# Kernel tuning notes

Hardware: AMD Instinct MI355X
Metric: run time of the kernel (lower is better)

The kernel has to match this reference:

```python
import jax, jax.numpy as jnp
import numpy as np

D_MODEL = 1024
D_STATE = 64
CHUNK = 256
BATCH = 4
SEQ_LEN = 4096


def setup_inputs() -> dict:
    key = jax.random.key(0)
    k1, k2, k3, k4, k5 = jax.random.split(key, 5)
    u = jax.random.normal(k1, (BATCH, SEQ_LEN, D_MODEL), jnp.float32)
    delta = jax.random.uniform(k2, (BATCH, SEQ_LEN, D_MODEL), jnp.float32)
    B = jax.random.normal(k3, (BATCH, SEQ_LEN, D_STATE), jnp.float32)
    C = jax.random.normal(k4, (BATCH, SEQ_LEN, D_STATE), jnp.float32)
    # matches nn.init.uniform_(A_log, -3.0, -1.0)
    A_log = jax.random.uniform(k5, (D_STATE, D_MODEL), jnp.float32, minval=-3.0, maxval=-1.0)
    return {"u": u, "delta": delta, "B": B, "C": C, "A_log": A_log}


def reference(u, delta, B, C, A_log):
    # delta is accepted but unused, as in the original forward.
    batch, seq_len, d_model = u.shape
    d_state = A_log.shape[0]
    n_chunks = seq_len // CHUNK  # seq_len chosen divisible by chunk_size
    A = -jnp.exp(A_log)  # (N, D)

    # Split sequence into chunks; hidden state resets at each chunk boundary,
    # so all chunks scan independently (vectorized over the n_chunks axis).
    # time-major layout for lax.scan: (CHUNK, batch, n_chunks, ...)
    uc = jnp.moveaxis(u.reshape(batch, n_chunks, CHUNK, d_model), 2, 0)
    Bc = jnp.moveaxis(B.reshape(batch, n_chunks, CHUNK, d_state), 2, 0)
    Cc = jnp.moveaxis(C.reshape(batch, n_chunks, CHUNK, d_state), 2, 0)

    h0 = jnp.zeros((batch, n_chunks, d_state, d_model), u.dtype)

    def step(h, inp):
        x_t, B_t, C_t = inp  # (b,c,D), (b,c,N), (b,c,N)
        h = A * h + B_t[..., :, None] * x_t[..., None, :]  # (b,c,N,D)
        y = jnp.einsum('bcn,bcnd->bcd', C_t, h)             # (b,c,D)
        return h, y

    _, ys = jax.lax.scan(step, h0, (uc, Bc, Cc))  # (CHUNK, b, n_chunks, D)
    out = jnp.moveaxis(ys, 0, 2).reshape(batch, seq_len, d_model)
    return out
```

## Files before the change

kernel.cpp:

```cpp
#include <hip/hip_runtime.h>

typedef float v4 __attribute__((ext_vector_type(4)));

#define D_MODEL 1024
#define D_STATE 64
#define CHUNK   256
#define TILE_T  64

__global__ __launch_bounds__(256, 4)
void YvParallelScan_kernel(const float* __restrict__ u,
                           const float* __restrict__ B,
                           const float* __restrict__ C,
                           const float* __restrict__ A_log,
                           float* __restrict__ out) {
    __shared__ v4 sB[TILE_T * 16];
    __shared__ v4 sC[TILE_T * 16];

    const int bid = blockIdx.x;
    const int bc  = bid >> 4;
    const int ds  = bid & 15;
    const int tid = threadIdx.x;
    const int ng  = tid & 3;
    const int dq  = tid >> 2;
    const int d   = ds * 64 + dq;
    const int rowbase = bc * CHUNK;

    const v4* Bg = (const v4*)(B + (size_t)rowbase * D_STATE);
    const v4* Cg = (const v4*)(C + (size_t)rowbase * D_STATE);

    float a[16], h[16];
#pragma unroll
    for (int j = 0; j < 16; ++j) {
        const int n = ng * 16 + j;
        a[j] = -__expf(A_log[n * D_MODEL + d]);
        h[j] = 0.f;
    }

    const float* uptr = u + (size_t)rowbase * D_MODEL + d;
    float*       optr = out + (size_t)rowbase * D_MODEL + d;

    float xa = uptr[0];
    float xb = uptr[D_MODEL];

    for (int ti = 0; ti < CHUNK / TILE_T; ++ti) {
#pragma unroll
        for (int k = 0; k < 4; ++k) {
            sB[k * 256 + tid] = Bg[ti * 1024 + k * 256 + tid];
            sC[k * 256 + tid] = Cg[ti * 1024 + k * 256 + tid];
        }
        __syncthreads();

#pragma unroll 4
        for (int tl = 0; tl < TILE_T; ++tl) {
            const int t  = ti * TILE_T + tl;
            const int tp = (t + 2 < CHUNK) ? (t + 2) : (CHUNK - 1);
            const float xn = uptr[(size_t)tp * D_MODEL];

            const float x = xa;
            float acc0 = 0.f, acc1 = 0.f;
#pragma unroll
            for (int jj = 0; jj < 4; ++jj) {
                const v4 b4 = sB[tl * 16 + ng * 4 + jj];
                const v4 c4 = sC[tl * 16 + ng * 4 + jj];
#pragma unroll
                for (int k = 0; k < 4; ++k) {
                    const int j = jj * 4 + k;
                    h[j] = a[j] * h[j] + b4[k] * x;
                    if (k & 1) acc1 += c4[k] * h[j];
                    else       acc0 += c4[k] * h[j];
                }
            }
            float acc = acc0 + acc1;
            acc += __shfl_xor(acc, 1);
            acc += __shfl_xor(acc, 2);
            if (ng == 0) optr[(size_t)t * D_MODEL] = acc;
            xa = xb; xb = xn;
        }
        __syncthreads();
    }
}

extern "C" void kernel_launch(void* const* d_in, const int* in_sizes, int n_in,
                              void* d_out, int out_size, void* d_ws, size_t ws_size,
                              hipStream_t stream) {
    const float* u     = (const float*)d_in[0];
    const float* B     = (const float*)d_in[2];
    const float* C     = (const float*)d_in[3];
    const float* A_log = (const float*)d_in[4];
    float* out = (float*)d_out;

    YvParallelScan_kernel<<<1024, 256, 0, stream>>>(u, B, C, A_log, out);
}
```

Baseline: 259.6 us.

## Process two d-channels per thread and stream B/C from registers instead of LDS

Each thread now handles two adjacent model channels, so every B/C element read is reused across two state recurrences. Shared-memory staging and block barriers are removed: B and C values are loaded straight from global memory into registers and double-buffered one timestep ahead. The grid is halved to 512 blocks and launch bounds drop to 2 waves-per-EU to fit the extra registers. This trades lower occupancy and fewer blocks (less parallelism across CUs) for fewer barriers, fewer LDS reads and vectorized u/out accesses.

```diff
diff --git a/kernel.cpp b/kernel.cpp
--- a/kernel.cpp
+++ b/kernel.cpp
@@ -1,82 +1,111 @@
 #include <hip/hip_runtime.h>
 
 typedef float v4 __attribute__((ext_vector_type(4)));
+typedef float v2 __attribute__((ext_vector_type(2)));
 
 #define D_MODEL 1024
 #define D_STATE 64
 #define CHUNK   256
-#define TILE_T  64
 
-__global__ __launch_bounds__(256, 4)
+__global__ __launch_bounds__(256, 2)
 void YvParallelScan_kernel(const float* __restrict__ u,
                            const float* __restrict__ B,
                            const float* __restrict__ C,
                            const float* __restrict__ A_log,
                            float* __restrict__ out) {
-    __shared__ v4 sB[TILE_T * 16];
-    __shared__ v4 sC[TILE_T * 16];
-
     const int bid = blockIdx.x;
-    const int bc  = bid >> 4;
-    const int ds  = bid & 15;
+    const int bc  = bid >> 3;
+    const int dsl = bid & 7;
     const int tid = threadIdx.x;
     const int ng  = tid & 3;
-    const int dq  = tid >> 2;
-    const int d   = ds * 64 + dq;
+    const int dp  = tid >> 2;
+    const int d   = dsl * 128 + dp * 2;
     const int rowbase = bc * CHUNK;
 
-    const v4* Bg = (const v4*)(B + (size_t)rowbase * D_STATE);
-    const v4* Cg = (const v4*)(C + (size_t)rowbase * D_STATE);
-
-    float a[16], h[16];
+    float a0[16], a1[16], h0[16], h1[16];
 #pragma unroll
     for (int j = 0; j < 16; ++j) {
         const int n = ng * 16 + j;
-        a[j] = -__expf(A_log[n * D_MODEL + d]);
-        h[j] = 0.f;
+        v2 al = *(const v2*)(A_log + (size_t)n * D_MODEL + d);
+        a0[j] = -__expf(al[0]);
+        a1[j] = -__expf(al[1]);
+        h0[j] = 0.f; h1[j] = 0.f;
     }
 
-    const float* uptr = u + (size_t)rowbase * D_MODEL + d;
+    const v4* Bg = (const v4*)(B + (size_t)rowbase * D_STATE) + ng * 4;
+    const v4* Cg = (const v4*)(C + (size_t)rowbase * D_STATE) + ng * 4;
+    const float* uptr = u   + (size_t)rowbase * D_MODEL + d;
     float*       optr = out + (size_t)rowbase * D_MODEL + d;
 
-    float xa = uptr[0];
-    float xb = uptr[D_MODEL];
+    v2 x0 = *(const v2*)(uptr);
+    v2 x1 = *(const v2*)(uptr + D_MODEL);
 
-    for (int ti = 0; ti < CHUNK / TILE_T; ++ti) {
+    v4 bA[4], cA[4], bB[4], cB[4];
 #pragma unroll
-        for (int k = 0; k < 4; ++k) {
-            sB[k * 256 + tid] = Bg[ti * 1024 + k * 256 + tid];
-            sC[k * 256 + tid] = Cg[ti * 1024 + k * 256 + tid];
-        }
-        __syncthreads();
+    for (int jj = 0; jj < 4; ++jj) { bA[jj] = Bg[jj]; cA[jj] = Cg[jj]; }
 
-#pragma unroll 4
-        for (int tl = 0; tl < TILE_T; ++tl) {
-            const int t  = ti * TILE_T + tl;
-            const int tp = (t + 2 < CHUNK) ? (t + 2) : (CHUNK - 1);
-            const float xn = uptr[(size_t)tp * D_MODEL];
+    for (int t = 0; t < CHUNK; t += 2) {
+        {
+#pragma unroll
+            for (int jj = 0; jj < 4; ++jj) {
+                bB[jj] = Bg[(size_t)(t + 1) * 16 + jj];
+                cB[jj] = Cg[(size_t)(t + 1) * 16 + jj];
+            }
+            const int tp = (t + 2 < CHUNK) ? t + 2 : CHUNK - 1;
+            const v2 xn = *(const v2*)(uptr + (size_t)tp * D_MODEL);
 
-            const float x = xa;
             float acc0 = 0.f, acc1 = 0.f;
 #pragma unroll
             for (int jj = 0; jj < 4; ++jj) {
-                const v4 b4 = sB[tl * 16 + ng * 4 + jj];
-                const v4 c4 = sC[tl * 16 + ng * 4 + jj];
+                const v4 b = bA[jj], c = cA[jj];
 #pragma unroll
                 for (int k = 0; k < 4; ++k) {
                     const int j = jj * 4 + k;
-                    h[j] = a[j] * h[j] + b4[k] * x;
-                    if (k & 1) acc1 += c4[k] * h[j];
-                    else       acc0 += c4[k] * h[j];
+                    h0[j] = a0[j] * h0[j] + b[k] * x0[0];
+                    h1[j] = a1[j] * h1[j] + b[k] * x0[1];
+                    acc0 += c[k] * h0[j];
+                    acc1 += c[k] * h1[j];
                 }
             }
-            float acc = acc0 + acc1;
-            acc += __shfl_xor(acc, 1);
-            acc += __shfl_xor(acc, 2);
-            if (ng == 0) optr[(size_t)t * D_MODEL] = acc;
-            xa = xb; xb = xn;
+            acc0 += __shfl_xor(acc0, 1); acc0 += __shfl_xor(acc0, 2);
+            acc1 += __shfl_xor(acc1, 1); acc1 += __shfl_xor(acc1, 2);
+            if (ng == 0) {
+                v2 o; o[0] = acc0; o[1] = acc1;
+                *(v2*)(optr + (size_t)t * D_MODEL) = o;
+            }
+            x0 = x1; x1 = xn;
         }
-        __syncthreads();
+        {
+            const int tn = (t + 2 < CHUNK) ? t + 2 : CHUNK - 1;
+#pragma unroll
+            for (int jj = 0; jj < 4; ++jj) {
+                bA[jj] = Bg[(size_t)tn * 16 + jj];
+                cA[jj] = Cg[(size_t)tn * 16 + jj];
+            }
+            const int tp = (t + 3 < CHUNK) ? t + 3 : CHUNK - 1;
+            const v2 xn = *(const v2*)(uptr + (size_t)tp * D_MODEL);
+
+            float acc0 = 0.f, acc1 = 0.f;
+#pragma unroll
+            for (int jj = 0; jj < 4; ++jj) {
+                const v4 b = bB[jj], c = cB[jj];
+#pragma unroll
+                for (int k = 0; k < 4; ++k) {
+                    const int j = jj * 4 + k;
+                    h0[j] = a0[j] * h0[j] + b[k] * x0[0];
+                    h1[j] = a1[j] * h1[j] + b[k] * x0[1];
+                    acc0 += c[k] * h0[j];
+                    acc1 += c[k] * h1[j];
+                }
+            }
+            acc0 += __shfl_xor(acc0, 1); acc0 += __shfl_xor(acc0, 2);
+            acc1 += __shfl_xor(acc1, 1); acc1 += __shfl_xor(acc1, 2);
+            if (ng == 0) {
+                v2 o; o[0] = acc0; o[1] = acc1;
+                *(v2*)(optr + (size_t)(t + 1) * D_MODEL) = o;
+            }
+            x0 = x1; x1 = xn;
+        }
     }
 }
 
@@ -89,5 +118,5 @@
     const float* A_log = (const float*)d_in[4];
     float* out = (float*)d_out;
 
-    YvParallelScan_kernel<<<1024, 256, 0, stream>>>(u, B, C, A_log, out);
+    YvParallelScan_kernel<<<512, 256, 0, stream>>>(u, B, C, A_log, out);
 }
```

Measured after the change: 378.6 us. +45.9%, slower.
